# Performance work log

Hardware: AMD Instinct MI355X
Metric: run time of the kernel (lower is better)

## Reference

```python
import jax, jax.numpy as jnp
import numpy as np

B, T, C = 2, 2048, 1024
H = 16
D = C // H
SCALE = 0.1 / (D ** 0.5)  # nonstandard 0.1/sqrt(head_dim) scale from source


def setup_inputs() -> dict:
    key = jax.random.key(0)
    ks = jax.random.split(key, 5)
    s = 0.02
    return {
        "x": jax.random.normal(ks[0], (B, T, C), jnp.float32),
        "w_attn": jax.random.normal(ks[1], (C, 3 * C), jnp.float32) * s,
        "b_attn": jax.random.normal(ks[2], (3 * C,), jnp.float32) * s,
        "w_proj": jax.random.normal(ks[3], (C, C), jnp.float32) * s,
        "b_proj": jax.random.normal(ks[4], (C,), jnp.float32) * s,
    }


def reference(x, w_attn, b_attn, w_proj, b_proj):
    Bs, Ts, Cs = x.shape
    qkv = x @ w_attn + b_attn                      # [B,T,3C]
    q, k, v = jnp.split(qkv, 3, axis=-1)
    q = q.reshape(Bs, Ts, H, D)                    # [B,T,H,D]
    k = k.reshape(Bs, Ts, H, D)
    v = v.reshape(Bs, Ts, H, D)
    attn = jnp.einsum("bthd,bshd->bhts", q, k) * SCALE  # [B,H,T,T]
    causal = jnp.tril(jnp.ones((Ts, Ts), dtype=bool))
    attn = jnp.where(causal, attn, -jnp.inf)
    attn = jax.nn.softmax(attn, axis=-1)
    y = jnp.einsum("bhts,bshd->bthd", attn, v).reshape(Bs, Ts, Cs)
    return y @ w_proj + b_proj
```

## Files before the change

### kernel.cpp

```cpp
#include <hip/hip_runtime.h>


#define Bz 2
#define Tz 2048
#define Cz 1024
#define Hz 16
#define Dz 64
#define QSCALE 0.01803368801111437f

typedef unsigned short u16;
typedef short bf16x8 __attribute__((ext_vector_type(8)));
typedef float f32x4 __attribute__((ext_vector_type(4)));

__device__ inline u16 f2bf(float f) {
  return (u16)((__float_as_uint(f) + 0x8000u) >> 16);
}

__device__ inline float fexp2(float x) {
#if __has_builtin(__builtin_amdgcn_exp2f)
  return __builtin_amdgcn_exp2f(x);
#else
  return exp2f(x);
#endif
}

__device__ inline void gl_lds16(const u16* g, u16* l) {
  __builtin_amdgcn_global_load_lds(
      (const __attribute__((address_space(1))) void*)g,
      (__attribute__((address_space(3))) void*)l, 16, 0, 0);
}

#define NCAST 4096
#define NTA   3072
__global__ __launch_bounds__(256) void prep_kernel(const float* __restrict__ x,
                                                   const float* __restrict__ wa,
                                                   const float* __restrict__ wp,
                                                   u16* __restrict__ xb,
                                                   u16* __restrict__ waT,
                                                   u16* __restrict__ wpT) {
  const int bx = blockIdx.x, t = threadIdx.x;
  if (bx < NCAST) {
    int i = bx * 256 + t;
    float4 v = ((const float4*)x)[i];
    ushort4 o = {f2bf(v.x), f2bf(v.y), f2bf(v.z), f2bf(v.w)};
    ((ushort4*)xb)[i] = o;
    return;
  }
  __shared__ float tile[32][33];
  const float* W;
  u16* WT;
  int N, idx;
  if (bx < NCAST + NTA) {
    W = wa; WT = waT; N = 3 * Cz; idx = bx - NCAST;
  } else {
    W = wp; WT = wpT; N = Cz; idx = bx - NCAST - NTA;
  }
  const int n0 = (idx % (N / 32)) * 32, k0 = (idx / (N / 32)) * 32;
  const int tx = t & 31, ty = t >> 5;
#pragma unroll
  for (int i = 0; i < 4; ++i)
    tile[ty + 8 * i][tx] = W[(size_t)(k0 + ty + 8 * i) * N + n0 + tx];
  __syncthreads();
#pragma unroll
  for (int i = 0; i < 4; ++i)
    WT[(size_t)(n0 + ty + 8 * i) * Cz + k0 + tx] = f2bf(tile[tx][ty + 8 * i]);
}

template <bool OUT_BF16, int TN>
__global__ __launch_bounds__(256) void gemm_bt(const u16* __restrict__ A,
                                               const u16* __restrict__ BT,
                                               const float* __restrict__ bias,
                                               void* __restrict__ Cout,
                                               int M, int N, int K,
                                               int qcols, float qscale) {
  __shared__ __align__(16) u16 As[128 * 32];
  __shared__ __align__(16) u16 Bs[TN * 32];
  constexpr int NT = TN / 32;
  const int t = threadIdx.x;
  const int wave = t >> 6, lane = t & 63;
  const int lm = lane & 15, lg = lane >> 4;
  const int wm = wave >> 1, wn = wave & 1;
  const int m0 = blockIdx.y * 128, n0 = blockIdx.x * TN;

  const int srow_in = lane >> 2;
  const int gseg = (lane & 3) ^ ((lane >> 3) & 3);
  const size_t a_off0 = (size_t)(m0 + 32 * wave + srow_in) * K + gseg * 8;
  const size_t a_off1 = a_off0 + 16 * (size_t)K;
  u16* asl0 = &As[(32 * wave) * 32];
  u16* asl1 = &As[(32 * wave + 16) * 32];
  size_t b_off0 = 0, b_off1 = 0;
  u16 *bsl0, *bsl1 = nullptr;
  if constexpr (TN == 128) {
    b_off0 = (size_t)(n0 + 32 * wave + srow_in) * K + gseg * 8;
    b_off1 = b_off0 + 16 * (size_t)K;
    bsl0 = &Bs[(32 * wave) * 32];
    bsl1 = &Bs[(32 * wave + 16) * 32];
  } else {
    b_off0 = (size_t)(n0 + 16 * wave + srow_in) * K + gseg * 8;
    bsl0 = &Bs[(16 * wave) * 32];
  }
  const int rseg = (lg ^ ((lm >> 1) & 3)) * 8;

  f32x4 acc[4][NT];
#pragma unroll
  for (int mt = 0; mt < 4; ++mt)
#pragma unroll
    for (int nt = 0; nt < NT; ++nt)
#pragma unroll
      for (int i = 0; i < 4; ++i) acc[mt][nt][i] = 0.f;

  for (int k0 = 0; k0 < K; k0 += 32) {
    __syncthreads();
    gl_lds16(A + a_off0 + k0, asl0);
    gl_lds16(A + a_off1 + k0, asl1);
    gl_lds16(BT + b_off0 + k0, bsl0);
    if constexpr (TN == 128) gl_lds16(BT + b_off1 + k0, bsl1);
    __syncthreads();

    bf16x8 af[4], bfr[NT];
#pragma unroll
    for (int mt = 0; mt < 4; ++mt)
      af[mt] = *(const bf16x8*)&As[(64 * wm + 16 * mt + lm) * 32 + rseg];
#pragma unroll
    for (int nt = 0; nt < NT; ++nt)
      bfr[nt] = *(const bf16x8*)&Bs[((TN / 2) * wn + 16 * nt + lm) * 32 + rseg];
#pragma unroll
    for (int mt = 0; mt < 4; ++mt)
#pragma unroll
      for (int nt = 0; nt < NT; ++nt)
        acc[mt][nt] = __builtin_amdgcn_mfma_f32_16x16x32_bf16(af[mt], bfr[nt],
                                                              acc[mt][nt], 0, 0, 0);
  }

#pragma unroll
  for (int nt = 0; nt < NT; ++nt) {
    int gc = n0 + (TN / 2) * wn + 16 * nt + lm;
    float bv = bias[gc];
    float sc = (gc < qcols) ? qscale : 1.f;
#pragma unroll
    for (int mt = 0; mt < 4; ++mt) {
#pragma unroll
      for (int i = 0; i < 4; ++i) {
        int gr = m0 + 64 * wm + 16 * mt + 4 * lg + i;
        float v = (acc[mt][nt][i] + bv) * sc;
        if (OUT_BF16)
          ((u16*)Cout)[(size_t)gr * N + gc] = f2bf(v);
        else
          ((float*)Cout)[(size_t)gr * N + gc] = v;
      }
    }
  }
}

__global__ __launch_bounds__(256) void attn_kernel(const u16* __restrict__ qkv,
                                                   u16* __restrict__ yb) {
  __shared__ __align__(16) u16 Ks[64][72];
  __shared__ __align__(16) u16 Vt[64][72];
  __shared__ __align__(16) u16 Ps[64][72];

  const int t = threadIdx.x;
  const int wave = t >> 6, lane = t & 63;
  const int lm = lane & 15, lg = lane >> 4;
  const int kg8 = lg << 3;
  const int x = blockIdx.x;
  const int bh = x & 31, qtp = x >> 5;
  const int qt = (qtp < 16) ? qtp : 47 - qtp;
  const int b = bh >> 4, h = bh & 15;
  const int q0 = qt * 64;
  const size_t rowstride = 3 * Cz;
  const u16* qbase = qkv + (size_t)b * Tz * rowstride + h * Dz;

  bf16x8 qf[2];
  {
    const u16* qrow = qbase + (size_t)(q0 + wave * 16 + lm) * rowstride + kg8;
    qf[0] = *(const bf16x8*)qrow;
    qf[1] = *(const bf16x8*)(qrow + 32);
  }

  float psum[4];
  f32x4 Oa[4];
#pragma unroll
  for (int i = 0; i < 4; ++i) {
    psum[i] = 0.f;
#pragma unroll
    for (int j = 0; j < 4; ++j) Oa[i][j] = 0.f;
  }

  const int ksr = t >> 2, kds = (t & 3) << 4;
  const int vsp = t & 31, vds = (t >> 5) << 3;
  const u16* kbase = qbase + Cz + (size_t)ksr * rowstride + kds;
  const u16* vbase = qbase + 2 * Cz + (size_t)(2 * vsp) * rowstride + vds;
  const size_t tilestep = 64 * rowstride;

  uint4 krA[2], vrA[2], krB[2], vrB[2];
  {
    const u16* kp = kbase;
    const u16* vp = vbase;
    krA[0] = *(const uint4*)kp;
    krA[1] = *(const uint4*)(kp + 8);
    vrA[0] = *(const uint4*)vp;
    vrA[1] = *(const uint4*)(vp + rowstride);
    const int t1 = (qt >= 1) ? 1 : 0;
    kp = kbase + (size_t)t1 * tilestep;
    vp = vbase + (size_t)t1 * tilestep;
    krB[0] = *(const uint4*)kp;
    krB[1] = *(const uint4*)(kp + 8);
    vrB[0] = *(const uint4*)vp;
    vrB[1] = *(const uint4*)(vp + rowstride);
  }

  auto stage = [&](uint4 (&kr)[2], uint4 (&vr)[2], int ktc) {
    __syncthreads();
    *(uint4*)&Ks[ksr][kds] = kr[0];
    *(uint4*)&Ks[ksr][kds + 8] = kr[1];
    {
      unsigned av[4] = {vr[0].x, vr[0].y, vr[0].z, vr[0].w};
      unsigned cv[4] = {vr[1].x, vr[1].y, vr[1].z, vr[1].w};
#pragma unroll
      for (int j = 0; j < 4; ++j) {
        unsigned w0 = (av[j] & 0xffffu) | (cv[j] << 16);
        unsigned w1 = (av[j] >> 16) | (cv[j] & 0xffff0000u);
        *(unsigned*)&Vt[vds + 2 * j][2 * vsp] = w0;
        *(unsigned*)&Vt[vds + 2 * j + 1][2 * vsp] = w1;
      }
    }
    __syncthreads();

    if (ktc + 2 <= qt) {
      const u16* kp = kbase + (size_t)(ktc + 2) * tilestep;
      const u16* vp = vbase + (size_t)(ktc + 2) * tilestep;
      kr[0] = *(const uint4*)kp;
      kr[1] = *(const uint4*)(kp + 8);
      vr[0] = *(const uint4*)vp;
      vr[1] = *(const uint4*)(vp + rowstride);
    }

    f32x4 S[4];
#pragma unroll
    for (int c = 0; c < 4; ++c) {
      bf16x8 k0 = *(const bf16x8*)&Ks[c * 16 + lm][kg8];
      bf16x8 k1 = *(const bf16x8*)&Ks[c * 16 + lm][32 + kg8];
      f32x4 s;
#pragma unroll
      for (int i = 0; i < 4; ++i) s[i] = 0.f;
      s = __builtin_amdgcn_mfma_f32_16x16x32_bf16(qf[0], k0, s, 0, 0, 0);
      s = __builtin_amdgcn_mfma_f32_16x16x32_bf16(qf[1], k1, s, 0, 0, 0);
      S[c] = s;
    }

    const bool diag = (ktc == qt);
#pragma unroll
    for (int c = 0; c < 4; ++c) {
#pragma unroll
      for (int r = 0; r < 4; ++r) {
        float p = fexp2(S[c][r]);
        if (diag && (c * 16 + lm) > (16 * wave + 4 * lg + r)) p = 0.f;
        psum[r] += p;
        Ps[16 * wave + 4 * lg + r][c * 16 + lm] = f2bf(p);
      }
    }

    bf16x8 pf0 = *(const bf16x8*)&Ps[16 * wave + lm][kg8];
    bf16x8 pf1 = *(const bf16x8*)&Ps[16 * wave + lm][32 + kg8];
#pragma unroll
    for (int c = 0; c < 4; ++c) {
      bf16x8 v0 = *(const bf16x8*)&Vt[c * 16 + lm][kg8];
      bf16x8 v1 = *(const bf16x8*)&Vt[c * 16 + lm][32 + kg8];
      Oa[c] = __builtin_amdgcn_mfma_f32_16x16x32_bf16(pf0, v0, Oa[c], 0, 0, 0);
      Oa[c] = __builtin_amdgcn_mfma_f32_16x16x32_bf16(pf1, v1, Oa[c], 0, 0, 0);
    }
  };

  for (int kt = 0; kt <= qt; kt += 2) {
    stage(krA, vrA, kt);
    if (kt + 1 <= qt) stage(krB, vrB, kt + 1);
  }

  float inv[4];
#pragma unroll
  for (int r = 0; r < 4; ++r) {
    float s = psum[r];
#pragma unroll
    for (int msk = 1; msk < 16; msk <<= 1) s += __shfl_xor(s, msk);
    inv[r] = 1.f / s;
  }
#pragma unroll
  for (int c = 0; c < 4; ++c)
#pragma unroll
    for (int r = 0; r < 4; ++r)
      Ps[16 * wave + 4 * lg + r][c * 16 + lm] = f2bf(Oa[c][r] * inv[r]);

  {
    const int row = lane >> 2, seg = lane & 3;
    const uint4* src = (const uint4*)&Ps[16 * wave + row][seg * 16];
    uint4 v0 = src[0];
    uint4 v1 = src[1];
    u16* dst = yb + (size_t)(b * Tz + q0 + 16 * wave + row) * Cz + h * Dz + seg * 16;
    *(uint4*)dst = v0;
    *(uint4*)(dst + 8) = v1;
  }
}

extern "C" void kernel_launch(void* const* d_in, const int* in_sizes, int n_in,
                              void* d_out, int out_size, void* d_ws, size_t ws_size,
                              hipStream_t stream) {
  const float* x      = (const float*)d_in[0];
  const float* w_attn = (const float*)d_in[1];
  const float* b_attn = (const float*)d_in[2];
  const float* w_proj = (const float*)d_in[3];
  const float* b_proj = (const float*)d_in[4];

  char* ws = (char*)d_ws;
  u16* xb   = (u16*)(ws);
  u16* waT  = (u16*)(ws + (8ull << 20));
  u16* wpT  = (u16*)(ws + (14ull << 20));
  u16* qkvb = (u16*)(ws + (16ull << 20));
  u16* yb   = (u16*)(ws + (40ull << 20));

  const int M = Bz * Tz;

  prep_kernel<<<NCAST + NTA + 1024, 256, 0, stream>>>(x, w_attn, w_proj, xb, waT, wpT);
  gemm_bt<true, 128><<<dim3(3 * Cz / 128, M / 128), 256, 0, stream>>>(
      xb, waT, b_attn, qkvb, M, 3 * Cz, Cz, Cz, QSCALE);
  attn_kernel<<<1024, 256, 0, stream>>>(qkvb, yb);
  gemm_bt<false, 64><<<dim3(Cz / 64, M / 128), 256, 0, stream>>>(
      yb, wpT, b_proj, d_out, M, Cz, Cz, 0, 1.f);
}
```

Measured before the change: 205.0 us.

## Process two query tiles per attention block and double-buffer K/V in LDS

```diff
diff --git a/kernel.cpp b/kernel.cpp
--- a/kernel.cpp
+++ b/kernel.cpp
@@ -154,8 +154,8 @@
 
 __global__ __launch_bounds__(256) void attn_kernel(const u16* __restrict__ qkv,
                                                    u16* __restrict__ yb) {
-  __shared__ __align__(16) u16 Ks[64][72];
-  __shared__ __align__(16) u16 Vt[64][72];
+  __shared__ __align__(16) u16 Ks[2][64][72];
+  __shared__ __align__(16) u16 Vt[2][64][72];
   __shared__ __align__(16) u16 Ps[64][72];
 
   const int t = threadIdx.x;
@@ -164,27 +164,31 @@
   const int kg8 = lg << 3;
   const int x = blockIdx.x;
   const int bh = x & 31, qtp = x >> 5;
-  const int qt = (qtp < 16) ? qtp : 47 - qtp;
+  const int qt = (qtp < 8) ? qtp : 23 - qtp;
   const int b = bh >> 4, h = bh & 15;
-  const int q0 = qt * 64;
+  const int q0 = qt * 128;
+  const int ktmax = 2 * qt + 1;
   const size_t rowstride = 3 * Cz;
   const u16* qbase = qkv + (size_t)b * Tz * rowstride + h * Dz;
 
-  bf16x8 qf[2];
-  {
-    const u16* qrow = qbase + (size_t)(q0 + wave * 16 + lm) * rowstride + kg8;
-    qf[0] = *(const bf16x8*)qrow;
-    qf[1] = *(const bf16x8*)(qrow + 32);
-  }
-
-  float psum[4];
-  f32x4 Oa[4];
-#pragma unroll
-  for (int i = 0; i < 4; ++i) {
-    psum[i] = 0.f;
-#pragma unroll
-    for (int j = 0; j < 4; ++j) Oa[i][j] = 0.f;
-  }
+  bf16x8 qf[2][2];
+#pragma unroll
+  for (int rt = 0; rt < 2; ++rt) {
+    const u16* qrow = qbase + (size_t)(q0 + 64 * rt + 16 * wave + lm) * rowstride + kg8;
+    qf[rt][0] = *(const bf16x8*)qrow;
+    qf[rt][1] = *(const bf16x8*)(qrow + 32);
+  }
+
+  float psum[2][4];
+  f32x4 Oa[2][4];
+#pragma unroll
+  for (int rt = 0; rt < 2; ++rt)
+#pragma unroll
+    for (int i = 0; i < 4; ++i) {
+      psum[rt][i] = 0.f;
+#pragma unroll
+      for (int j = 0; j < 4; ++j) Oa[rt][i][j] = 0.f;
+    }
 
   const int ksr = t >> 2, kds = (t & 3) << 4;
   const int vsp = t & 31, vds = (t >> 5) << 3;
@@ -192,110 +196,109 @@
   const u16* vbase = qbase + 2 * Cz + (size_t)(2 * vsp) * rowstride + vds;
   const size_t tilestep = 64 * rowstride;
 
-  uint4 krA[2], vrA[2], krB[2], vrB[2];
-  {
-    const u16* kp = kbase;
-    const u16* vp = vbase;
-    krA[0] = *(const uint4*)kp;
-    krA[1] = *(const uint4*)(kp + 8);
-    vrA[0] = *(const uint4*)vp;
-    vrA[1] = *(const uint4*)(vp + rowstride);
-    const int t1 = (qt >= 1) ? 1 : 0;
-    kp = kbase + (size_t)t1 * tilestep;
-    vp = vbase + (size_t)t1 * tilestep;
-    krB[0] = *(const uint4*)kp;
-    krB[1] = *(const uint4*)(kp + 8);
-    vrB[0] = *(const uint4*)vp;
-    vrB[1] = *(const uint4*)(vp + rowstride);
-  }
-
-  auto stage = [&](uint4 (&kr)[2], uint4 (&vr)[2], int ktc) {
+  auto load_tile = [&](int kt, uint4 (&kr)[2], uint4 (&vr)[2]) {
+    const u16* kp = kbase + (size_t)kt * tilestep;
+    const u16* vp = vbase + (size_t)kt * tilestep;
+    kr[0] = *(const uint4*)kp;
+    kr[1] = *(const uint4*)(kp + 8);
+    vr[0] = *(const uint4*)vp;
+    vr[1] = *(const uint4*)(vp + rowstride);
+  };
+  auto stage_write = [&](int buf, const uint4 (&kr)[2], const uint4 (&vr)[2]) {
+    *(uint4*)&Ks[buf][ksr][kds] = kr[0];
+    *(uint4*)&Ks[buf][ksr][kds + 8] = kr[1];
+    unsigned av[4] = {vr[0].x, vr[0].y, vr[0].z, vr[0].w};
+    unsigned cv[4] = {vr[1].x, vr[1].y, vr[1].z, vr[1].w};
+#pragma unroll
+    for (int j = 0; j < 4; ++j) {
+      unsigned w0 = (av[j] & 0xffffu) | (cv[j] << 16);
+      unsigned w1 = (av[j] >> 16) | (cv[j] & 0xffff0000u);
+      *(unsigned*)&Vt[buf][vds + 2 * j][2 * vsp] = w0;
+      *(unsigned*)&Vt[buf][vds + 2 * j + 1][2 * vsp] = w1;
+    }
+  };
+
+  uint4 kr[2], vr[2];
+  load_tile(0, kr, vr);
+  stage_write(0, kr, vr);
+  load_tile(1, kr, vr);
+
+  for (int kt = 0; kt <= ktmax; ++kt) {
     __syncthreads();
-    *(uint4*)&Ks[ksr][kds] = kr[0];
-    *(uint4*)&Ks[ksr][kds + 8] = kr[1];
-    {
-      unsigned av[4] = {vr[0].x, vr[0].y, vr[0].z, vr[0].w};
-      unsigned cv[4] = {vr[1].x, vr[1].y, vr[1].z, vr[1].w};
-#pragma unroll
-      for (int j = 0; j < 4; ++j) {
-        unsigned w0 = (av[j] & 0xffffu) | (cv[j] << 16);
-        unsigned w1 = (av[j] >> 16) | (cv[j] & 0xffff0000u);
-        *(unsigned*)&Vt[vds + 2 * j][2 * vsp] = w0;
-        *(unsigned*)&Vt[vds + 2 * j + 1][2 * vsp] = w1;
+    if (kt + 1 <= ktmax) {
+      stage_write((kt + 1) & 1, kr, vr);
+      if (kt + 2 <= ktmax) load_tile(kt + 2, kr, vr);
+    }
+    const int cb = kt & 1;
+
+    bf16x8 kf0[4], kf1[4], vf0[4], vf1[4];
+#pragma unroll
+    for (int c = 0; c < 4; ++c) {
+      kf0[c] = *(const bf16x8*)&Ks[cb][c * 16 + lm][kg8];
+      kf1[c] = *(const bf16x8*)&Ks[cb][c * 16 + lm][32 + kg8];
+      vf0[c] = *(const bf16x8*)&Vt[cb][c * 16 + lm][kg8];
+      vf1[c] = *(const bf16x8*)&Vt[cb][c * 16 + lm][32 + kg8];
+    }
+
+#pragma unroll
+    for (int rt = 0; rt < 2; ++rt) {
+      if (kt > 2 * qt + rt) continue;
+      const bool diag = (kt == 2 * qt + rt);
+
+      f32x4 S[4];
+#pragma unroll
+      for (int c = 0; c < 4; ++c) {
+        f32x4 s;
+#pragma unroll
+        for (int i = 0; i < 4; ++i) s[i] = 0.f;
+        s = __builtin_amdgcn_mfma_f32_16x16x32_bf16(qf[rt][0], kf0[c], s, 0, 0, 0);
+        s = __builtin_amdgcn_mfma_f32_16x16x32_bf16(qf[rt][1], kf1[c], s, 0, 0, 0);
+        S[c] = s;
       }
-    }
-    __syncthreads();
-
-    if (ktc + 2 <= qt) {
-      const u16* kp = kbase + (size_t)(ktc + 2) * tilestep;
-      const u16* vp = vbase + (size_t)(ktc + 2) * tilestep;
-      kr[0] = *(const uint4*)kp;
-      kr[1] = *(const uint4*)(kp + 8);
-      vr[0] = *(const uint4*)vp;
-      vr[1] = *(const uint4*)(vp + rowstride);
-    }
-
-    f32x4 S[4];
-#pragma unroll
-    for (int c = 0; c < 4; ++c) {
-      bf16x8 k0 = *(const bf16x8*)&Ks[c * 16 + lm][kg8];
-      bf16x8 k1 = *(const bf16x8*)&Ks[c * 16 + lm][32 + kg8];
-      f32x4 s;
-#pragma unroll
-      for (int i = 0; i < 4; ++i) s[i] = 0.f;
-      s = __builtin_amdgcn_mfma_f32_16x16x32_bf16(qf[0], k0, s, 0, 0, 0);
-      s = __builtin_amdgcn_mfma_f32_16x16x32_bf16(qf[1], k1, s, 0, 0, 0);
-      S[c] = s;
-    }
-
-    const bool diag = (ktc == qt);
-#pragma unroll
-    for (int c = 0; c < 4; ++c) {
-#pragma unroll
-      for (int r = 0; r < 4; ++r) {
-        float p = fexp2(S[c][r]);
-        if (diag && (c * 16 + lm) > (16 * wave + 4 * lg + r)) p = 0.f;
-        psum[r] += p;
-        Ps[16 * wave + 4 * lg + r][c * 16 + lm] = f2bf(p);
+
+#pragma unroll
+      for (int c = 0; c < 4; ++c) {
+#pragma unroll
+        for (int r = 0; r < 4; ++r) {
+          float p = fexp2(S[c][r]);
+          if (diag && (c * 16 + lm) > (16 * wave + 4 * lg + r)) p = 0.f;
+          psum[rt][r] += p;
+          Ps[16 * wave + 4 * lg + r][c * 16 + lm] = f2bf(p);
+        }
       }
-    }
-
-    bf16x8 pf0 = *(const bf16x8*)&Ps[16 * wave + lm][kg8];
-    bf16x8 pf1 = *(const bf16x8*)&Ps[16 * wave + lm][32 + kg8];
-#pragma unroll
-    for (int c = 0; c < 4; ++c) {
-      bf16x8 v0 = *(const bf16x8*)&Vt[c * 16 + lm][kg8];
-      bf16x8 v1 = *(const bf16x8*)&Vt[c * 16 + lm][32 + kg8];
-      Oa[c] = __builtin_amdgcn_mfma_f32_16x16x32_bf16(pf0, v0, Oa[c], 0, 0, 0);
-      Oa[c] = __builtin_amdgcn_mfma_f32_16x16x32_bf16(pf1, v1, Oa[c], 0, 0, 0);
-    }
-  };
-
-  for (int kt = 0; kt <= qt; kt += 2) {
-    stage(krA, vrA, kt);
-    if (kt + 1 <= qt) stage(krB, vrB, kt + 1);
-  }
-
-  float inv[4];
-#pragma unroll
-  for (int r = 0; r < 4; ++r) {
-    float s = psum[r];
-#pragma unroll
-    for (int msk = 1; msk < 16; msk <<= 1) s += __shfl_xor(s, msk);
-    inv[r] = 1.f / s;
-  }
-#pragma unroll
-  for (int c = 0; c < 4; ++c)
-#pragma unroll
-    for (int r = 0; r < 4; ++r)
-      Ps[16 * wave + 4 * lg + r][c * 16 + lm] = f2bf(Oa[c][r] * inv[r]);
-
-  {
+
+      bf16x8 pf0 = *(const bf16x8*)&Ps[16 * wave + lm][kg8];
+      bf16x8 pf1 = *(const bf16x8*)&Ps[16 * wave + lm][32 + kg8];
+#pragma unroll
+      for (int c = 0; c < 4; ++c) {
+        Oa[rt][c] = __builtin_amdgcn_mfma_f32_16x16x32_bf16(pf0, vf0[c], Oa[rt][c], 0, 0, 0);
+        Oa[rt][c] = __builtin_amdgcn_mfma_f32_16x16x32_bf16(pf1, vf1[c], Oa[rt][c], 0, 0, 0);
+      }
+    }
+  }
+
+#pragma unroll
+  for (int rt = 0; rt < 2; ++rt) {
+    float inv[4];
+#pragma unroll
+    for (int r = 0; r < 4; ++r) {
+      float s = psum[rt][r];
+#pragma unroll
+      for (int msk = 1; msk < 16; msk <<= 1) s += __shfl_xor(s, msk);
+      inv[r] = 1.f / s;
+    }
+#pragma unroll
+    for (int c = 0; c < 4; ++c)
+#pragma unroll
+      for (int r = 0; r < 4; ++r)
+        Ps[16 * wave + 4 * lg + r][c * 16 + lm] = f2bf(Oa[rt][c][r] * inv[r]);
+
     const int row = lane >> 2, seg = lane & 3;
     const uint4* src = (const uint4*)&Ps[16 * wave + row][seg * 16];
     uint4 v0 = src[0];
     uint4 v1 = src[1];
-    u16* dst = yb + (size_t)(b * Tz + q0 + 16 * wave + row) * Cz + h * Dz + seg * 16;
+    u16* dst = yb + (size_t)(b * Tz + q0 + 64 * rt + 16 * wave + row) * Cz +
+               h * Dz + seg * 16;
     *(uint4*)dst = v0;
     *(uint4*)(dst + 8) = v1;
   }
@@ -322,7 +325,7 @@
   prep_kernel<<<NCAST + NTA + 1024, 256, 0, stream>>>(x, w_attn, w_proj, xb, waT, wpT);
   gemm_bt<true, 128><<<dim3(3 * Cz / 128, M / 128), 256, 0, stream>>>(
       xb, waT, b_attn, qkvb, M, 3 * Cz, Cz, Cz, QSCALE);
-  attn_kernel<<<1024, 256, 0, stream>>>(qkvb, yb);
+  attn_kernel<<<512, 256, 0, stream>>>(qkvb, yb);
   gemm_bt<false, 64><<<dim3(Cz / 64, M / 128), 256, 0, stream>>>(
       yb, wpT, b_proj, d_out, M, Cz, Cz, 0, 1.f);
 }
```

After: 212.6 us. +3.7%, slower.
